# Optimization experiments

Measured on AMD Instinct MI355X. Metric: run time of the kernel, lower is better.

## Reference

```python
import jax, jax.numpy as jnp
import numpy as np

V, E, H, B, S, L = 32000, 512, 1024, 128, 256, 2


def setup_inputs() -> dict:
    key = jax.random.key(0)
    ks = jax.random.split(key, 20)
    sc = 0.02
    n = lambda k, shape: jax.random.normal(k, shape, dtype=jnp.float32) * sc
    return {
        "input_ids": jax.random.randint(ks[0], (B,), 0, V),
        "h0": jax.random.normal(ks[1], (L, B, H), dtype=jnp.float32),
        "c0": jax.random.normal(ks[2], (L, B, H), dtype=jnp.float32),
        "enc_out": jax.random.normal(ks[3], (S, B, H), dtype=jnp.float32),
        "emb": n(ks[4], (V, E)),
        "w_ih0": n(ks[5], (4 * H, E)),
        "w_hh0": n(ks[6], (4 * H, H)),
        "b_ih0": n(ks[7], (4 * H,)),
        "b_hh0": n(ks[8], (4 * H,)),
        "w_ih1": n(ks[9], (4 * H, H)),
        "w_hh1": n(ks[10], (4 * H, H)),
        "b_ih1": n(ks[11], (4 * H,)),
        "b_hh1": n(ks[12], (4 * H,)),
        "attn_w": n(ks[13], (H, H)),
        "attn_b": n(ks[14], (H,)),
        "concat_w": n(ks[15], (H, 2 * H)),
        "concat_b": n(ks[16], (H,)),
        "out_w": n(ks[17], (V, H)),
        "out_b": n(ks[18], (V,)),
    }


def _lstm_step(x, h, c, w_ih, w_hh, b_ih, b_hh):
    # PyTorch gate order: i, f, g, o
    g = x @ w_ih.T + b_ih + h @ w_hh.T + b_hh  # [B, 4H]
    i, f, gg, o = jnp.split(g, 4, axis=-1)
    c_new = jax.nn.sigmoid(f) * c + jax.nn.sigmoid(i) * jnp.tanh(gg)
    h_new = jax.nn.sigmoid(o) * jnp.tanh(c_new)
    return h_new, c_new


def reference(input_ids, h0, c0, enc_out, emb, w_ih0, w_hh0, b_ih0, b_hh0,
              w_ih1, w_hh1, b_ih1, b_hh1, attn_w, attn_b, concat_w, concat_b,
              out_w, out_b):
    x = emb[input_ids]  # [B, E] (dropout is identity in eval)
    h_0, c_0 = _lstm_step(x, h0[0], c0[0], w_ih0, w_hh0, b_ih0, b_hh0)
    h_1, c_1 = _lstm_step(h_0, h0[1], c0[1], w_ih1, w_hh1, b_ih1, b_hh1)
    rnn_out = h_1  # [B, H] == rnn_output.squeeze(0)
    # Luong general attention: scores[b,s] = <W enc[s,b], rnn_out[b]>
    e_proj = enc_out @ attn_w.T + attn_b          # [S, B, H]
    scores = jnp.einsum('sbh,bh->bs', e_proj, rnn_out)  # [B, S]
    attn = jax.nn.softmax(scores, axis=-1)
    context = jnp.einsum('bs,sbh->bh', attn, enc_out)   # [B, H]
    concat_out = jnp.tanh(
        jnp.concatenate([rnn_out, context], axis=-1) @ concat_w.T + concat_b)
    logits = concat_out @ out_w.T + out_b         # [B, V]
    h_new = jnp.stack([h_0, h_1])
    c_new = jnp.stack([c_0, c_1])
    return logits, h_new, c_new
```

## Files before the change

kernel.cpp:

```cpp
#include <hip/hip_runtime.h>
#include <hip/hip_bf16.h>
#include <cstddef>
#include <cstdint>

constexpr int Bv = 128;
constexpr int Sv = 256;
constexpr int Hv = 1024;
constexpr int Ev = 512;
constexpr int Vv = 32000;

typedef __attribute__((ext_vector_type(4))) float f32x4;
typedef __attribute__((ext_vector_type(8))) short short8;

__device__ __forceinline__ uint2 cvt4(float4 v) {
  union { __hip_bfloat162 b; unsigned u; } lo, hi;
  lo.b = __float22bfloat162_rn(float2{v.x, v.y});
  hi.b = __float22bfloat162_rn(float2{v.z, v.w});
  uint2 r;
  r.x = lo.u;
  r.y = hi.u;
  return r;
}
__device__ __forceinline__ unsigned short cvt1(float x) {
  union { __hip_bfloat16 b; unsigned short u; } c;
  c.b = __float2bfloat16(x);
  return c.u;
}

template <int BM, int BN, int BK, int SPLIT, int WTR, int GATHER, int MINW>
__global__ __launch_bounds__(256, MINW) void gemm_mfma(
    const int* __restrict__ ids,
    const float* __restrict__ A1, int lda1, int K1,
    const float* __restrict__ A2, int lda2, int K2,
    const float* __restrict__ W1, int ldw1,
    const float* __restrict__ W2, int ldw2,
    const float* __restrict__ bias1, const float* __restrict__ bias2,
    float* __restrict__ C, int ldc, int N) {
  constexpr int LP = BK + 8;
  constexpr int KQ = BK / 4;
  constexpr int KSUB = BK / 32;
  constexpr int WAVES_N = (BN >= 64) ? 2 : 1;
  constexpr int WAVES_M = 4 / WAVES_N;
  constexpr int WM = BM / WAVES_M;
  constexpr int FM = WM / 16;
  constexpr int FN = 2;
  constexpr int ACH = (BM * BK) / (4 * 256);
  constexpr int WCH = (BN * BK) / (4 * 256);
  constexpr int WVN = WTR ? (BK * 8 / 256) : WCH;

  __shared__ unsigned short Al[BM * LP];
  __shared__ unsigned short Wl[BN * LP];

  const int tid = threadIdx.x;
  const int wid = tid >> 6, lane = tid & 63;
  const int nBlock = blockIdx.x * BN;
  const int mBlock = blockIdx.y * BM;
  const int z = blockIdx.z;
  int wm, wn;
  if (WAVES_N == 2) { wm = (wid >> 1) * WM; wn = (wid & 1) * 32; }
  else              { wm = wid * WM;        wn = 0; }

  float4 av[ACH], wv[WVN];

  auto load_tile = [&](int kg) {
    const bool seg1 = kg < K1;
    const float* Wseg = seg1 ? W1 : W2;
    const int ldw = seg1 ? ldw1 : ldw2;
    const int kloc = seg1 ? kg : kg - K1;
#pragma unroll
    for (int i = 0; i < ACH; i++) {
      int c = tid + i * 256;
      int m = c / KQ, kq = (c % KQ) * 4;
      const float* arow;
      if (seg1) {
        if (GATHER) arow = A1 + (size_t)ids[mBlock + m] * lda1;
        else        arow = A1 + (size_t)(mBlock + m) * lda1;
      } else {
        arow = A2 + (size_t)(mBlock + m) * lda2;
      }
      av[i] = *(const float4*)(arow + kloc + kq);
    }
    if (WTR) {
#pragma unroll
      for (int i = 0; i < WVN; i++) {
        int c = tid + i * 256;
        int row = c >> 3, colq = c & 7;
        wv[i] = *(const float4*)(Wseg + (size_t)(kloc + row) * ldw + nBlock + colq * 4);
      }
    } else {
#pragma unroll
      for (int i = 0; i < WCH; i++) {
        int c = tid + i * 256;
        int n = c / KQ, kq = (c % KQ) * 4;
        wv[i] = *(const float4*)(Wseg + (size_t)(nBlock + n) * ldw + kloc + kq);
      }
    }
  };

  const int KT = K1 + K2;
  const int KS = KT / SPLIT;
  const int kbeg = z * KS;
  const int NS = KS / BK;
  load_tile(kbeg);
  f32x4 acc[FM][FN] = {};

  for (int step = 0; step < NS; ++step) {
    __syncthreads();
#pragma unroll
    for (int i = 0; i < ACH; i++) {
      int c = tid + i * 256;
      int m = c / KQ, kq = (c % KQ) * 4;
      *(uint2*)&Al[m * LP + kq] = cvt4(av[i]);
    }
    if (WTR) {
#pragma unroll
      for (int i = 0; i < WVN; i++) {
        int c = tid + i * 256;
        int row = c >> 3, colq = c & 7;
        Wl[(colq * 4 + 0) * LP + row] = cvt1(wv[i].x);
        Wl[(colq * 4 + 1) * LP + row] = cvt1(wv[i].y);
        Wl[(colq * 4 + 2) * LP + row] = cvt1(wv[i].z);
        Wl[(colq * 4 + 3) * LP + row] = cvt1(wv[i].w);
      }
    } else {
#pragma unroll
      for (int i = 0; i < WCH; i++) {
        int c = tid + i * 256;
        int n = c / KQ, kq = (c % KQ) * 4;
        *(uint2*)&Wl[n * LP + kq] = cvt4(wv[i]);
      }
    }
    __syncthreads();

    if (step + 1 < NS) load_tile(kbeg + (step + 1) * BK);

    const int klane = (lane >> 4) << 3;
    const int r = lane & 15;
    short8 af[KSUB][FM], wf[KSUB][FN];
#pragma unroll
    for (int ks = 0; ks < KSUB; ks++) {
#pragma unroll
      for (int f = 0; f < FM; f++)
        af[ks][f] = *(const short8*)&Al[(wm + f * 16 + r) * LP + ks * 32 + klane];
#pragma unroll
      for (int f = 0; f < FN; f++)
        wf[ks][f] = *(const short8*)&Wl[(wn + f * 16 + r) * LP + ks * 32 + klane];
    }
#pragma unroll
    for (int ks = 0; ks < KSUB; ks++)
#pragma unroll
      for (int fm = 0; fm < FM; fm++)
#pragma unroll
        for (int fn = 0; fn < FN; fn++)
          acc[fm][fn] = __builtin_amdgcn_mfma_f32_16x16x32_bf16(
              af[ks][fm], wf[ks][fn], acc[fm][fn], 0, 0, 0);
  }

  float* Cp = C + (size_t)z * gridDim.y * BM * ldc;
  const int col = lane & 15, rb = (lane >> 4) << 2;
#pragma unroll
  for (int fn = 0; fn < FN; fn++) {
    int n = nBlock + wn + fn * 16 + col;
    float bsum = 0.f;
    if (z == 0) {
      if (bias1) bsum += bias1[n];
      if (bias2) bsum += bias2[n];
    }
#pragma unroll
    for (int fm = 0; fm < FM; fm++) {
#pragma unroll
      for (int j = 0; j < 4; j++) {
        int m = mBlock + wm + fm * 16 + rb + j;
        Cp[(size_t)m * ldc + n] = acc[fm][fn][j] + bsum;
      }
    }
  }
}

template <int P>
__global__ void lstm_pw(const float* __restrict__ Gp,
                        const float* __restrict__ c_prev,
                        float* __restrict__ h_out,
                        float* __restrict__ c_out) {
  int i4 = blockIdx.x * 256 + threadIdx.x;
  int b = i4 >> 8, j4 = i4 & 255;
  float4 gi{}, gf{}, gg{}, go{};
#pragma unroll
  for (int p = 0; p < P; p++) {
    const float4* g = (const float4*)(Gp + (size_t)p * Bv * 4 * Hv + (size_t)b * 4096);
    float4 a = g[j4], bb = g[256 + j4], c = g[512 + j4], d = g[768 + j4];
    gi.x += a.x; gi.y += a.y; gi.z += a.z; gi.w += a.w;
    gf.x += bb.x; gf.y += bb.y; gf.z += bb.z; gf.w += bb.w;
    gg.x += c.x; gg.y += c.y; gg.z += c.z; gg.w += c.w;
    go.x += d.x; go.y += d.y; go.z += d.z; go.w += d.w;
  }
  float4 c4 = ((const float4*)c_prev)[i4];
  float4 h4, cn4;
  float* gip = &gi.x; float* gfp = &gf.x; float* ggp = &gg.x; float* gop = &go.x;
  float* cp = &c4.x; float* hp = &h4.x; float* cnp = &cn4.x;
#pragma unroll
  for (int u = 0; u < 4; u++) {
    float si = 1.f / (1.f + expf(-gip[u]));
    float sf = 1.f / (1.f + expf(-gfp[u]));
    float so = 1.f / (1.f + expf(-gop[u]));
    float cn = sf * cp[u] + si * tanhf(ggp[u]);
    hp[u] = so * tanhf(cn);
    cnp[u] = cn;
  }
  ((float4*)h_out)[i4] = h4;
  ((float4*)c_out)[i4] = cn4;
}

__global__ void scores_k(const float* __restrict__ enc,
                         const float* __restrict__ qp,
                         float* __restrict__ sc) {
  int blk = blockIdx.x;
  int b = blk >> 6, s4 = blk & 63;
  int t = threadIdx.x;
  __shared__ float qs[1024];
  {
    const float4* q0 = (const float4*)(qp + (size_t)b * Hv);
    const float4* q1 = (const float4*)(qp + 1 * Bv * Hv + (size_t)b * Hv);
    const float4* q2 = (const float4*)(qp + 2 * Bv * Hv + (size_t)b * Hv);
    const float4* q3 = (const float4*)(qp + 3 * Bv * Hv + (size_t)b * Hv);
    float4 a = q0[t], bq = q1[t], c = q2[t], d = q3[t];
    float4 s;
    s.x = a.x + bq.x + c.x + d.x; s.y = a.y + bq.y + c.y + d.y;
    s.z = a.z + bq.z + c.z + d.z; s.w = a.w + bq.w + c.w + d.w;
    ((float4*)qs)[t] = s;
  }
  __syncthreads();
  int wid = t >> 6, lane = t & 63;
  int s = s4 * 4 + wid;
  const float4* e4 = (const float4*)(enc + ((size_t)s * Bv + b) * Hv);
  const float4* q4 = (const float4*)qs;
  float sum = 0.f;
#pragma unroll
  for (int i = 0; i < 4; i++) {
    int idx = lane + i * 64;
    float4 e = e4[idx], qq = q4[idx];
    sum += e.x * qq.x + e.y * qq.y + e.z * qq.z + e.w * qq.w;
  }
#pragma unroll
  for (int o = 32; o; o >>= 1) sum += __shfl_xor(sum, o);
  if (lane == 0) sc[(size_t)b * Sv + s] = sum;
}

__global__ void context_k(const float* __restrict__ sc_in,
                          const float* __restrict__ enc,
                          float* __restrict__ ctx) {
  int blk = blockIdx.x;
  int b = blk >> 2, hc = (blk & 3) * 256;
  int t = threadIdx.x, lane = t & 63;
  __shared__ float a[256];
  __shared__ float redm[4], reds[4];
  float v = sc_in[(size_t)b * Sv + t];
  float m = v;
#pragma unroll
  for (int o = 32; o; o >>= 1) m = fmaxf(m, __shfl_xor(m, o));
  if (lane == 0) redm[t >> 6] = m;
  __syncthreads();
  m = fmaxf(fmaxf(redm[0], redm[1]), fmaxf(redm[2], redm[3]));
  float e = expf(v - m);
  float ssum = e;
#pragma unroll
  for (int o = 32; o; o >>= 1) ssum += __shfl_xor(ssum, o);
  if (lane == 0) reds[t >> 6] = ssum;
  __syncthreads();
  ssum = (reds[0] + reds[1]) + (reds[2] + reds[3]);
  a[t] = e / ssum;
  __syncthreads();

  float acc = 0.f;
  const float* ebase = enc + (size_t)b * Hv + hc + t;
#pragma unroll 8
  for (int s = 0; s < Sv; s++)
    acc += a[s] * ebase[(size_t)s * Bv * Hv];
  ctx[(size_t)b * Hv + hc + t] = acc;
}

__global__ void finish_cat(const float* __restrict__ catp,
                           float* __restrict__ cat) {
  int i4 = blockIdx.x * 256 + threadIdx.x;
  constexpr int ST = Bv * Hv / 4;
  const float4* p = (const float4*)catp;
  float4 a = p[i4], b = p[ST + i4], c = p[2 * ST + i4], d = p[3 * ST + i4];
  float4 r;
  r.x = tanhf(a.x + b.x + c.x + d.x);
  r.y = tanhf(a.y + b.y + c.y + d.y);
  r.z = tanhf(a.z + b.z + c.z + d.z);
  r.w = tanhf(a.w + b.w + c.w + d.w);
  ((float4*)cat)[i4] = r;
}

extern "C" void kernel_launch(void* const* d_in, const int* in_sizes, int n_in,
                              void* d_out, int out_size, void* d_ws,
                              size_t ws_size, hipStream_t stream) {
  const int*   ids      = (const int*)d_in[0];
  const float* h0       = (const float*)d_in[1];
  const float* c0       = (const float*)d_in[2];
  const float* enc      = (const float*)d_in[3];
  const float* emb      = (const float*)d_in[4];
  const float* w_ih0    = (const float*)d_in[5];
  const float* w_hh0    = (const float*)d_in[6];
  const float* b_ih0    = (const float*)d_in[7];
  const float* b_hh0    = (const float*)d_in[8];
  const float* w_ih1    = (const float*)d_in[9];
  const float* w_hh1    = (const float*)d_in[10];
  const float* b_ih1    = (const float*)d_in[11];
  const float* b_hh1    = (const float*)d_in[12];
  const float* attn_w   = (const float*)d_in[13];
  const float* attn_b   = (const float*)d_in[14];
  const float* concat_w = (const float*)d_in[15];
  const float* concat_b = (const float*)d_in[16];
  const float* out_w    = (const float*)d_in[17];
  const float* out_b    = (const float*)d_in[18];
  (void)attn_b;

  float* logits = (float*)d_out;
  float* hout   = logits + (size_t)Bv * Vv;
  float* cout   = hout + 2 * Bv * Hv;

  float* ws   = (float*)d_ws;
  float* G0p  = ws;
  float* G1p  = G0p + 3 * 524288;
  float* qp   = G1p + 4 * (size_t)524288;
  float* catp = qp + 4 * 131072;
  float* cat  = catp + 4 * 131072;
  float* ctx  = cat + 131072;
  float* sc   = ctx + 131072;

  const float* h_b = hout + Bv * Hv;

  gemm_mfma<64, 32, 64, 3, 0, 1, 4><<<dim3(128, 2, 3), 256, 0, stream>>>(
      ids, emb, Ev, Ev, h0, Hv, Hv, w_ih0, Ev, w_hh0, Hv, b_ih0, b_hh0,
      G0p, 4 * Hv, 4 * Hv);
  lstm_pw<3><<<128, 256, 0, stream>>>(G0p, c0, hout, cout);
  gemm_mfma<64, 32, 64, 4, 0, 0, 4><<<dim3(128, 2, 4), 256, 0, stream>>>(
      nullptr, hout, Hv, Hv, h0 + Bv * Hv, Hv, Hv, w_ih1, Hv, w_hh1, Hv,
      b_ih1, b_hh1, G1p, 4 * Hv, 4 * Hv);
  lstm_pw<4><<<128, 256, 0, stream>>>(G1p, c0 + Bv * Hv, hout + Bv * Hv,
                                      cout + Bv * Hv);
  gemm_mfma<64, 32, 64, 4, 1, 0, 4><<<dim3(32, 2, 4), 256, 0, stream>>>(
      nullptr, h_b, Hv, Hv, nullptr, 0, 0, attn_w, Hv,
      nullptr, 0, nullptr, nullptr, qp, Hv, Hv);
  scores_k<<<8192, 256, 0, stream>>>(enc, qp, sc);
  context_k<<<512, 256, 0, stream>>>(sc, enc, ctx);
  gemm_mfma<64, 32, 64, 4, 0, 0, 4><<<dim3(32, 2, 4), 256, 0, stream>>>(
      nullptr, h_b, Hv, Hv, ctx, Hv, Hv, concat_w, 2 * Hv,
      concat_w + Hv, 2 * Hv, concat_b, nullptr, catp, Hv, Hv);
  finish_cat<<<128, 256, 0, stream>>>(catp, cat);
  gemm_mfma<64, 64, 64, 1, 0, 0, 4><<<dim3(500, 2, 1), 256, 0, stream>>>(
      nullptr, cat, Hv, Hv, nullptr, 0, 0, out_w, Hv, nullptr, 0,
      out_b, nullptr, logits, Vv, Vv);
}
```

Measured before the change: 157.8 us.

## Swizzle output GEMM blocks and restructure scores/context kernels for wider loads

The vocab projection GEMM now uses a 1D grid with a grouped swizzle, so the two M-tiles sharing the same out_w columns are scheduled next to each other and the weight tile is reused from L2. The scores kernel computes four sequence positions per wave, which cuts the grid size and reuses the query values held in registers. The context kernel switches to float4 loads, splits the S dimension across waves and reduces the partial sums through shared memory. In exchange, the swizzle launches a few excess blocks that exit early, and the context reduction adds an extra barrier.

Result: slower. 165.5 us (+4.9%).

```diff
diff --git a/kernel.cpp b/kernel.cpp
--- a/kernel.cpp
+++ b/kernel.cpp
@@ -27,7 +27,8 @@
   return c.u;
 }
 
-template <int BM, int BN, int BK, int SPLIT, int WTR, int GATHER, int MINW>
+template <int BM, int BN, int BK, int SPLIT, int WTR, int GATHER, int LSWZ,
+          int MINW>
 __global__ __launch_bounds__(256, MINW) void gemm_mfma(
     const int* __restrict__ ids,
     const float* __restrict__ A1, int lda1, int K1,
@@ -53,8 +54,19 @@
 
   const int tid = threadIdx.x;
   const int wid = tid >> 6, lane = tid & 63;
-  const int nBlock = blockIdx.x * BN;
-  const int mBlock = blockIdx.y * BM;
+  int nBlock, mBlock;
+  if (LSWZ) {
+    int bid = blockIdx.x;
+    int g = bid >> 4, w = bid & 15;
+    int nIdx = g * 8 + (w & 7);
+    int mIdx = w >> 3;
+    if (nIdx * BN >= N) return;
+    nBlock = nIdx * BN;
+    mBlock = mIdx * BM;
+  } else {
+    nBlock = blockIdx.x * BN;
+    mBlock = blockIdx.y * BM;
+  }
   const int z = blockIdx.z;
   int wm, wn;
   if (WAVES_N == 2) { wm = (wid >> 1) * WM; wn = (wid & 1) * 32; }
@@ -215,7 +227,7 @@
                          const float* __restrict__ qp,
                          float* __restrict__ sc) {
   int blk = blockIdx.x;
-  int b = blk >> 6, s4 = blk & 63;
+  int b = blk >> 4, s16 = blk & 15;
   int t = threadIdx.x;
   __shared__ float qs[1024];
   {
@@ -231,19 +243,26 @@
   }
   __syncthreads();
   int wid = t >> 6, lane = t & 63;
-  int s = s4 * 4 + wid;
-  const float4* e4 = (const float4*)(enc + ((size_t)s * Bv + b) * Hv);
+  int s0 = s16 * 16 + wid * 4;
   const float4* q4 = (const float4*)qs;
-  float sum = 0.f;
-#pragma unroll
-  for (int i = 0; i < 4; i++) {
-    int idx = lane + i * 64;
-    float4 e = e4[idx], qq = q4[idx];
-    sum += e.x * qq.x + e.y * qq.y + e.z * qq.z + e.w * qq.w;
-  }
-#pragma unroll
-  for (int o = 32; o; o >>= 1) sum += __shfl_xor(sum, o);
-  if (lane == 0) sc[(size_t)b * Sv + s] = sum;
+  float sum[4] = {0.f, 0.f, 0.f, 0.f};
+#pragma unroll
+  for (int j = 0; j < 4; j++) {
+    int idx = lane + j * 64;
+    float4 qq = q4[idx];
+#pragma unroll
+    for (int i = 0; i < 4; i++) {
+      float4 e = *(const float4*)(enc + ((size_t)(s0 + i) * Bv + b) * Hv + idx * 4);
+      sum[i] += e.x * qq.x + e.y * qq.y + e.z * qq.z + e.w * qq.w;
+    }
+  }
+#pragma unroll
+  for (int i = 0; i < 4; i++)
+#pragma unroll
+    for (int o = 32; o; o >>= 1) sum[i] += __shfl_xor(sum[i], o);
+  if (lane == 0)
+    *(float4*)(sc + (size_t)b * Sv + s0) =
+        make_float4(sum[0], sum[1], sum[2], sum[3]);
 }
 
 __global__ void context_k(const float* __restrict__ sc_in,
@@ -251,7 +270,7 @@
                           float* __restrict__ ctx) {
   int blk = blockIdx.x;
   int b = blk >> 2, hc = (blk & 3) * 256;
-  int t = threadIdx.x, lane = t & 63;
+  int t = threadIdx.x, lane = t & 63, wid = t >> 6;
   __shared__ float a[256];
   __shared__ float redm[4], reds[4];
   float v = sc_in[(size_t)b * Sv + t];
@@ -271,12 +290,27 @@
   a[t] = e / ssum;
   __syncthreads();
 
-  float acc = 0.f;
-  const float* ebase = enc + (size_t)b * Hv + hc + t;
+  float4 acc = make_float4(0.f, 0.f, 0.f, 0.f);
+  const float* ebase = enc + (size_t)b * Hv + hc + lane * 4;
 #pragma unroll 8
-  for (int s = 0; s < Sv; s++)
-    acc += a[s] * ebase[(size_t)s * Bv * Hv];
-  ctx[(size_t)b * Hv + hc + t] = acc;
+  for (int s = wid * 64; s < wid * 64 + 64; s++) {
+    float4 e = *(const float4*)(ebase + (size_t)s * Bv * Hv);
+    float w = a[s];
+    acc.x += w * e.x; acc.y += w * e.y; acc.z += w * e.z; acc.w += w * e.w;
+  }
+  __shared__ float4 part[4][64];
+  part[wid][lane] = acc;
+  __syncthreads();
+  if (wid == 0) {
+    float4 p0 = part[0][lane], p1 = part[1][lane];
+    float4 p2 = part[2][lane], p3 = part[3][lane];
+    float4 r;
+    r.x = (p0.x + p1.x) + (p2.x + p3.x);
+    r.y = (p0.y + p1.y) + (p2.y + p3.y);
+    r.z = (p0.z + p1.z) + (p2.z + p3.z);
+    r.w = (p0.w + p1.w) + (p2.w + p3.w);
+    *(float4*)(ctx + (size_t)b * Hv + hc + lane * 4) = r;
+  }
 }
 
 __global__ void finish_cat(const float* __restrict__ catp,
@@ -332,25 +366,25 @@
 
   const float* h_b = hout + Bv * Hv;
 
-  gemm_mfma<64, 32, 64, 3, 0, 1, 4><<<dim3(128, 2, 3), 256, 0, stream>>>(
+  gemm_mfma<64, 32, 64, 3, 0, 1, 0, 4><<<dim3(128, 2, 3), 256, 0, stream>>>(
       ids, emb, Ev, Ev, h0, Hv, Hv, w_ih0, Ev, w_hh0, Hv, b_ih0, b_hh0,
       G0p, 4 * Hv, 4 * Hv);
   lstm_pw<3><<<128, 256, 0, stream>>>(G0p, c0, hout, cout);
-  gemm_mfma<64, 32, 64, 4, 0, 0, 4><<<dim3(128, 2, 4), 256, 0, stream>>>(
+  gemm_mfma<64, 32, 64, 4, 0, 0, 0, 4><<<dim3(128, 2, 4), 256, 0, stream>>>(
       nullptr, hout, Hv, Hv, h0 + Bv * Hv, Hv, Hv, w_ih1, Hv, w_hh1, Hv,
       b_ih1, b_hh1, G1p, 4 * Hv, 4 * Hv);
   lstm_pw<4><<<128, 256, 0, stream>>>(G1p, c0 + Bv * Hv, hout + Bv * Hv,
                                       cout + Bv * Hv);
-  gemm_mfma<64, 32, 64, 4, 1, 0, 4><<<dim3(32, 2, 4), 256, 0, stream>>>(
+  gemm_mfma<64, 32, 64, 4, 1, 0, 0, 4><<<dim3(32, 2, 4), 256, 0, stream>>>(
       nullptr, h_b, Hv, Hv, nullptr, 0, 0, attn_w, Hv,
       nullptr, 0, nullptr, nullptr, qp, Hv, Hv);
-  scores_k<<<8192, 256, 0, stream>>>(enc, qp, sc);
+  scores_k<<<2048, 256, 0, stream>>>(enc, qp, sc);
   context_k<<<512, 256, 0, stream>>>(sc, enc, ctx);
-  gemm_mfma<64, 32, 64, 4, 0, 0, 4><<<dim3(32, 2, 4), 256, 0, stream>>>(
+  gemm_mfma<64, 32, 64, 4, 0, 0, 0, 4><<<dim3(32, 2, 4), 256, 0, stream>>>(
       nullptr, h_b, Hv, Hv, ctx, Hv, Hv, concat_w, 2 * Hv,
       concat_w + Hv, 2 * Hv, concat_b, nullptr, catp, Hv, Hv);
   finish_cat<<<128, 256, 0, stream>>>(catp, cat);
-  gemm_mfma<64, 64, 64, 1, 0, 0, 4><<<dim3(500, 2, 1), 256, 0, stream>>>(
+  gemm_mfma<64, 64, 64, 1, 0, 0, 1, 4><<<dim3(1008, 1, 1), 256, 0, stream>>>(
       nullptr, cat, Hv, Hv, nullptr, 0, 0, out_w, Hv, nullptr, 0,
       out_b, nullptr, logits, Vv, Vv);
 }
```
